# Performance work log

Measured on AMD Instinct MI355X. Metric: run time of the kernel, lower is better.

The kernel has to match this reference:

```python
import jax, jax.numpy as jnp
import numpy as np

N = 50000          # nodes
E = 800000         # edges per meta-path (avg degree 16)
M = 2              # meta-paths
IN = 256           # in_size
H, D = 4, 64       # heads, out_size per head
HD = H * D
SEM_HID = 128      # SemanticAttention hidden_size
NEG_SLOPE = 0.2    # DGL GATConv default LeakyReLU slope


def setup_inputs() -> dict:
    key = jax.random.key(0)
    ks = jax.random.split(key, 10)
    h = jax.random.normal(ks[0], (N, IN), dtype=jnp.float32)
    src = jax.random.randint(ks[1], (M, E), 0, N, dtype=jnp.int32)
    dst = jax.random.randint(ks[2], (M, E), 0, N, dtype=jnp.int32)
    # per-meta-path GATConv params
    W = jax.random.normal(ks[3], (M, IN, HD), dtype=jnp.float32) * (1.0 / np.sqrt(IN))
    attn_l = jax.random.normal(ks[4], (M, H, D), dtype=jnp.float32) * 0.1
    attn_r = jax.random.normal(ks[5], (M, H, D), dtype=jnp.float32) * 0.1
    # semantic attention params
    sem_w1 = jax.random.normal(ks[6], (HD, SEM_HID), dtype=jnp.float32) * (1.0 / np.sqrt(HD))
    sem_b1 = jnp.zeros((SEM_HID,), dtype=jnp.float32)
    sem_w2 = jax.random.normal(ks[7], (SEM_HID, 1), dtype=jnp.float32) * (1.0 / np.sqrt(SEM_HID))
    return {"h": h, "src": src, "dst": dst, "W": W, "attn_l": attn_l,
            "attn_r": attn_r, "sem_w1": sem_w1, "sem_b1": sem_b1, "sem_w2": sem_w2}


def _gat_conv(h, s, d, W_i, al, ar):
    # h: [N, IN]; s, d: [E] int edge endpoints; returns [N, H*D]
    feat = (h @ W_i).reshape(N, H, D)                       # [N,H,D]
    el = jnp.einsum('nhd,hd->nh', feat, al)                 # [N,H]
    er = jnp.einsum('nhd,hd->nh', feat, ar)                 # [N,H]
    e = jax.nn.leaky_relu(el[s] + er[d], NEG_SLOPE)         # [E,H]
    # edge softmax over incoming edges of each dst node
    m = jax.ops.segment_max(e, d, num_segments=N)           # [N,H]
    m = jax.lax.stop_gradient(jnp.where(jnp.isfinite(m), m, 0.0))
    ex = jnp.exp(e - m[d])                                  # [E,H]
    den = jax.ops.segment_sum(ex, d, num_segments=N)        # [N,H]
    alpha = ex / jnp.maximum(den[d], 1e-9)                  # [E,H]
    msg = alpha[:, :, None] * feat[s]                       # [E,H,D]
    rst = jax.ops.segment_sum(msg, d, num_segments=N)       # [N,H,D] (zero for 0-in-degree)
    return jax.nn.elu(rst).reshape(N, HD)


def reference(h, src, dst, W, attn_l, attn_r, sem_w1, sem_b1, sem_w2):
    embs = [_gat_conv(h, src[i], dst[i], W[i], attn_l[i], attn_r[i]) for i in range(M)]
    z = jnp.stack(embs, axis=1)                             # [N,M,HD]
    # semantic attention: w = mean over nodes of MLP score per meta-path
    w = jnp.einsum('nms,so->mo', jnp.tanh(jnp.einsum('nmd,ds->nms', z, sem_w1) + sem_b1), sem_w2) / N  # [M,1]
    beta = jax.nn.softmax(w, axis=0)                        # [M,1]
    return jnp.einsum('nmd,mo->nd', z, beta)                # [N,HD]
```

## Files before the change

kernel.cpp:

```cpp
#include <hip/hip_runtime.h>
#include <hip/hip_bf16.h>

#define NND 50000
#define NE 800000
#define NM 2
#define INF 256
#define NH 4
#define HDIM 256
#define SHID 128
#define SLOPE 0.2f
#define NB 196
#define NREP 8

typedef unsigned short u16;
typedef __attribute__((ext_vector_type(8))) short bf16x8;
typedef __attribute__((ext_vector_type(4))) float f32x4;

__device__ __forceinline__ float us2f(u16 u) {
  union { unsigned int i; float f; } v; v.i = ((unsigned int)u) << 16; return v.f;
}
__device__ __forceinline__ u16 f2us(float f) {
  union { float f; unsigned int i; } v; v.f = f;
  unsigned int r = v.i + 0x7FFFu + ((v.i >> 16) & 1u);
  return (u16)(r >> 16);
}

#define GLDS(g, l) __builtin_amdgcn_global_load_lds( \
    (const __attribute__((address_space(1))) unsigned int*)(g), \
    (__attribute__((address_space(3))) unsigned int*)(l), 16, 0, 0)

__global__ __launch_bounds__(256) void kprep(
    const float* __restrict__ h, u16* __restrict__ hb,
    const float* __restrict__ W, u16* __restrict__ Wt,
    const float* __restrict__ w1, u16* __restrict__ w1t)
{
  __shared__ u16 tile[64][65];
  const int t = threadIdx.x;
  const int bid = blockIdx.x;
  if (bid < 6250) {
    const size_t i = ((size_t)bid * 256 + t) * 8;
    float4 a = *(const float4*)(h + i);
    float4 b = *(const float4*)(h + i + 4);
    bf16x8 r;
    r[0] = f2us(a.x); r[1] = f2us(a.y); r[2] = f2us(a.z); r[3] = f2us(a.w);
    r[4] = f2us(b.x); r[5] = f2us(b.y); r[6] = f2us(b.z); r[7] = f2us(b.w);
    *(bf16x8*)(hb + i) = r;
  } else if (bid < 6250 + 32) {
    const int b = bid - 6250;
    const int k0 = (b & 3) * 64, n0 = ((b >> 2) & 3) * 64;
    const float* Wm = W + (size_t)(b >> 4) * 65536;
    u16* Wtm = Wt + (size_t)(b >> 4) * 65536;
    const int lr = t >> 2, c0 = (t & 3) * 16;
#pragma unroll
    for (int i = 0; i < 16; ++i)
      tile[lr][c0 + i] = f2us(Wm[(size_t)(k0 + lr) * 256 + n0 + c0 + i]);
    __syncthreads();
#pragma unroll
    for (int i = 0; i < 16; ++i)
      Wtm[(size_t)(n0 + lr) * 256 + k0 + c0 + i] = tile[c0 + i][lr];
  } else {
    const int b = bid - 6282;
    const int k0 = (b & 3) * 64, j0 = (b >> 2) * 64;
    const int lr = t >> 2, c0 = (t & 3) * 16;
#pragma unroll
    for (int i = 0; i < 16; ++i)
      tile[lr][c0 + i] = f2us(w1[(size_t)(k0 + lr) * SHID + j0 + c0 + i]);
    __syncthreads();
#pragma unroll
    for (int i = 0; i < 16; ++i)
      w1t[(size_t)(j0 + lr) * 256 + k0 + c0 + i] = tile[c0 + i][lr];
  }
}

__global__ __launch_bounds__(256) void kc_hist_both(const int* __restrict__ dst_all,
                                                    int* __restrict__ hrep) {
  int e = blockIdx.x * 256 + threadIdx.x;
  int p = (e >= NE) ? 1 : 0;
  int rep = blockIdx.x & (NREP - 1);
  atomicAdd(hrep + ((size_t)p * NREP + rep) * (NND + 1) + dst_all[e] + 1, 1);
}

__global__ __launch_bounds__(256) void ks1(const int* __restrict__ hrep,
                                           int* __restrict__ rowptr,
                                           int* __restrict__ bsum) {
  __shared__ int wsums[4];
  const int t = threadIdx.x;
  const int p = blockIdx.x / NB, lb = blockIdx.x % NB;
  int* rp = rowptr + (size_t)p * (NND + 1);
  const int i = lb * 256 + t + 1;
  int v = 0;
  if (i <= NND) {
    const int* hp = hrep + (size_t)p * NREP * (NND + 1);
#pragma unroll
    for (int r = 0; r < NREP; ++r) v += hp[(size_t)r * (NND + 1) + i];
  }
  const int lane = t & 63, wid = t >> 6;
#pragma unroll
  for (int o = 1; o < 64; o <<= 1) {
    int u = __shfl_up(v, o, 64);
    if (lane >= o) v += u;
  }
  if (lane == 63) wsums[wid] = v;
  __syncthreads();
  if (t == 0) {
    int s = 0;
#pragma unroll
    for (int w = 0; w < 4; ++w) { int x = wsums[w]; wsums[w] = s; s += x; }
    bsum[blockIdx.x] = s;
  }
  __syncthreads();
  v += wsums[wid];
  if (i <= NND) rp[i] = v;
}

__global__ __launch_bounds__(256) void ks3(int* __restrict__ rowptr,
                                           const int* __restrict__ bsum,
                                           int* __restrict__ cursor) {
  __shared__ int redp[4];
  __shared__ int off_s;
  const int t = threadIdx.x;
  const int p = blockIdx.x / NB, lb = blockIdx.x % NB;
  int* rp = rowptr + (size_t)p * (NND + 1);
  int* cp = cursor + (size_t)p * NND;
  int partial = (t < lb) ? bsum[p * NB + t] : 0;
  const int lane = t & 63, wid = t >> 6;
#pragma unroll
  for (int o = 32; o; o >>= 1) partial += __shfl_xor(partial, o, 64);
  if (lane == 0) redp[wid] = partial;
  __syncthreads();
  if (t == 0) off_s = redp[0] + redp[1] + redp[2] + redp[3];
  __syncthreads();
  const int off = off_s;
  const int i = lb * 256 + t + 1;
  if (i <= NND) {
    int v = rp[i] + off;
    rp[i] = v;
    if (i < NND) cp[i] = v;
    if (i == 1) { cp[0] = 0; rp[0] = 0; }
  }
}

__global__ __launch_bounds__(256) void kc_scatter(
    const int* __restrict__ src, const int* __restrict__ dst,
    int* __restrict__ cursor, int* __restrict__ col,
    const float* __restrict__ el, const float* __restrict__ er,
    float* __restrict__ exps)
{
  int e = blockIdx.x * 256 + threadIdx.x;
  if (e >= NE) return;
  int s = src[e], d = dst[e];
  int pos = atomicAdd(cursor + d, 1);
  col[pos] = s;
  float4 a = *(const float4*)(el + s * 4);
  float4 b = *(const float4*)(er + d * 4);
  float4 r;
  float x;
  x = a.x + b.x; x = x > 0.f ? x : SLOPE * x; r.x = __expf(x);
  x = a.y + b.y; x = x > 0.f ? x : SLOPE * x; r.y = __expf(x);
  x = a.z + b.z; x = x > 0.f ? x : SLOPE * x; r.z = __expf(x);
  x = a.w + b.w; x = x > 0.f ? x : SLOPE * x; r.w = __expf(x);
  *(float4*)(exps + (size_t)pos * 4) = r;
}

__global__ __launch_bounds__(256) void k1_mfma(
    const u16* __restrict__ hb, const u16* __restrict__ Wt,
    const float* __restrict__ al, const float* __restrict__ ar,
    u16* __restrict__ feat, float* __restrict__ el, float* __restrict__ er)
{
  __shared__ u16 As[128 * 64];
  __shared__ u16 Bs[128 * 64];
  const int t = threadIdx.x;
  const int lane = t & 63;
  const int w = t >> 6;
  const int wr = w >> 1, wc = w & 1;
  const int row0 = blockIdx.x * 128;
  const int col0 = blockIdx.y * 128;

  const int srow = t >> 3;
  const int sg   = t & 7;
  const int sgl  = (sg ^ (srow & 7)) * 8;

  int ra[4], cb[4];
#pragma unroll
  for (int q = 0; q < 4; ++q) {
    int r = row0 + q * 32 + srow; if (r >= NND) r = NND - 1;
    ra[q] = r;
    cb[q] = col0 + q * 32 + srow;
  }

  f32x4 acc[4][4];
#pragma unroll
  for (int i = 0; i < 4; ++i)
#pragma unroll
    for (int j = 0; j < 4; ++j) acc[i][j] = (f32x4){0.f, 0.f, 0.f, 0.f};

  for (int ks = 0; ks < 4; ++ks) {
    const int kb = ks * 64 + sgl;
    __syncthreads();
#pragma unroll
    for (int q = 0; q < 4; ++q) {
      GLDS(hb + (size_t)ra[q] * INF + kb, As + q * 2048 + w * 512);
      GLDS(Wt + (size_t)cb[q] * 256 + kb, Bs + q * 2048 + w * 512);
    }
    __syncthreads();
#pragma unroll
    for (int kk = 0; kk < 2; ++kk) {
      bf16x8 af[4], bfr[4];
#pragma unroll
      for (int mi = 0; mi < 4; ++mi) {
        const int R = wr * 64 + mi * 16 + (lane & 15);
        const int g = kk * 4 + (lane >> 4);
        af[mi] = *(const bf16x8*)(As + R * 64 + (g ^ (R & 7)) * 8);
      }
#pragma unroll
      for (int ni = 0; ni < 4; ++ni) {
        const int R = wc * 64 + ni * 16 + (lane & 15);
        const int g = kk * 4 + (lane >> 4);
        bfr[ni] = *(const bf16x8*)(Bs + R * 64 + (g ^ (R & 7)) * 8);
      }
#pragma unroll
      for (int mi = 0; mi < 4; ++mi)
#pragma unroll
        for (int ni = 0; ni < 4; ++ni)
          acc[mi][ni] = __builtin_amdgcn_mfma_f32_16x16x32_bf16(af[mi], bfr[ni], acc[mi][ni], 0, 0, 0);
    }
  }
  const int head = (col0 >> 6) + wc;
  float alc[4], arc[4];
#pragma unroll
  for (int ni = 0; ni < 4; ++ni) {
    const int c = col0 + wc * 64 + ni * 16 + (lane & 15);
    alc[ni] = al[c]; arc[ni] = ar[c];
  }
#pragma unroll
  for (int mi = 0; mi < 4; ++mi) {
#pragma unroll
    for (int i = 0; i < 4; ++i) {
      const int r = row0 + wr * 64 + mi * 16 + (lane >> 4) * 4 + i;
      const bool valid = (r < NND);
      float pel = 0.f, per = 0.f;
#pragma unroll
      for (int ni = 0; ni < 4; ++ni) {
        const float fe = acc[mi][ni][i];
        if (valid)
          feat[(size_t)r * HDIM + col0 + wc * 64 + ni * 16 + (lane & 15)] = f2us(fe);
        pel = fmaf(fe, alc[ni], pel);
        per = fmaf(fe, arc[ni], per);
      }
#pragma unroll
      for (int o = 1; o < 16; o <<= 1) {
        pel += __shfl_xor(pel, o, 64);
        per += __shfl_xor(per, o, 64);
      }
      if (valid && (lane & 15) == 0) {
        el[r * 4 + head] = pel;
        er[r * 4 + head] = per;
      }
    }
  }
}

template<int OBF>
__global__ __launch_bounds__(256) void k3_gather(
    const int* __restrict__ rowptr, const int* __restrict__ col,
    const float* __restrict__ exps,
    const u16* __restrict__ feat, void* __restrict__ z)
{
  const int d = blockIdx.x * 4 + (threadIdx.x >> 6);
  if (d >= NND) return;
  const int lane = threadIdx.x & 63;
  const int h = lane >> 4;
  const int sub = lane & 15;
  const int beg = rowptr[d], end = rowptr[d + 1];

  float den = 0.f;
  for (int j = beg + sub; j < end; j += 16)
    den += exps[(size_t)j * 4 + h];
#pragma unroll
  for (int o = 1; o < 16; o <<= 1) den += __shfl_xor(den, o, 64);
  const float inv = 1.f / fmaxf(den, 1e-9f);

  float a0 = 0.f, a1 = 0.f, a2 = 0.f, a3 = 0.f;
  int j = beg;
  for (; j + 3 < end; j += 4) {
    int s0 = col[j], s1 = col[j + 1], s2 = col[j + 2], s3 = col[j + 3];
    float p0 = exps[(size_t)j * 4 + h] * inv;
    float p1 = exps[(size_t)(j + 1) * 4 + h] * inv;
    float p2 = exps[(size_t)(j + 2) * 4 + h] * inv;
    float p3 = exps[(size_t)(j + 3) * 4 + h] * inv;
    const ushort4 f0 = *(const ushort4*)(feat + (size_t)s0 * HDIM + lane * 4);
    const ushort4 f1 = *(const ushort4*)(feat + (size_t)s1 * HDIM + lane * 4);
    const ushort4 f2 = *(const ushort4*)(feat + (size_t)s2 * HDIM + lane * 4);
    const ushort4 f3 = *(const ushort4*)(feat + (size_t)s3 * HDIM + lane * 4);
    a0 = fmaf(p0, us2f(f0.x), a0); a1 = fmaf(p0, us2f(f0.y), a1);
    a2 = fmaf(p0, us2f(f0.z), a2); a3 = fmaf(p0, us2f(f0.w), a3);
    a0 = fmaf(p1, us2f(f1.x), a0); a1 = fmaf(p1, us2f(f1.y), a1);
    a2 = fmaf(p1, us2f(f1.z), a2); a3 = fmaf(p1, us2f(f1.w), a3);
    a0 = fmaf(p2, us2f(f2.x), a0); a1 = fmaf(p2, us2f(f2.y), a1);
    a2 = fmaf(p2, us2f(f2.z), a2); a3 = fmaf(p2, us2f(f2.w), a3);
    a0 = fmaf(p3, us2f(f3.x), a0); a1 = fmaf(p3, us2f(f3.y), a1);
    a2 = fmaf(p3, us2f(f3.z), a2); a3 = fmaf(p3, us2f(f3.w), a3);
  }
  for (; j < end; ++j) {
    int s = col[j];
    float p = exps[(size_t)j * 4 + h] * inv;
    const ushort4 f4 = *(const ushort4*)(feat + (size_t)s * HDIM + lane * 4);
    a0 = fmaf(p, us2f(f4.x), a0); a1 = fmaf(p, us2f(f4.y), a1);
    a2 = fmaf(p, us2f(f4.z), a2); a3 = fmaf(p, us2f(f4.w), a3);
  }
  a0 = a0 > 0.f ? a0 : expf(a0) - 1.f;
  a1 = a1 > 0.f ? a1 : expf(a1) - 1.f;
  a2 = a2 > 0.f ? a2 : expf(a2) - 1.f;
  a3 = a3 > 0.f ? a3 : expf(a3) - 1.f;
  const size_t idx = (size_t)d * HDIM + lane * 4;
  if (OBF) {
    ushort4 r; r.x = f2us(a0); r.y = f2us(a1); r.z = f2us(a2); r.w = f2us(a3);
    *(ushort4*)((u16*)z + idx) = r;
  } else {
    float4 r; r.x = a0; r.y = a1; r.z = a2; r.w = a3;
    *(float4*)((float*)z + idx) = r;
  }
}

template<int ZBF>
__global__ __launch_bounds__(256) void k4_mfma(
    const void* __restrict__ zsrc, const u16* __restrict__ w1t,
    const float* __restrict__ b1, const float* __restrict__ w2,
    float* __restrict__ wsum, int midx)
{
  __shared__ u16 As[128 * 64];
  __shared__ u16 Bs[128 * 64];
  __shared__ float red[4];
  const int t = threadIdx.x;
  const int lane = t & 63;
  const int w = t >> 6;
  const int wr = w >> 1, wc = w & 1;
  const int row0 = blockIdx.x * 128;
  const int srow = t >> 3;
  const int sg   = t & 7;
  const int sgl  = (sg ^ (srow & 7)) * 8;

  int ra[4], cb[4];
#pragma unroll
  for (int q = 0; q < 4; ++q) {
    int r = row0 + q * 32 + srow; if (r >= NND) r = NND - 1;
    ra[q] = r;
    cb[q] = q * 32 + srow;
  }

  f32x4 acc[4][4];
#pragma unroll
  for (int i = 0; i < 4; ++i)
#pragma unroll
    for (int j = 0; j < 4; ++j) acc[i][j] = (f32x4){0.f, 0.f, 0.f, 0.f};

  for (int ks = 0; ks < 4; ++ks) {
    const int kb = ks * 64 + sgl;
    __syncthreads();
    if (ZBF) {
#pragma unroll
      for (int q = 0; q < 4; ++q)
        GLDS((const u16*)zsrc + (size_t)ra[q] * HDIM + kb, As + q * 2048 + w * 512);
    } else {
      const float* zf = (const float*)zsrc;
#pragma unroll
      for (int q = 0; q < 4; ++q) {
        float4 a = *(const float4*)(zf + (size_t)ra[q] * HDIM + kb);
        float4 b = *(const float4*)(zf + (size_t)ra[q] * HDIM + kb + 4);
        bf16x8 r;
        r[0] = f2us(a.x); r[1] = f2us(a.y); r[2] = f2us(a.z); r[3] = f2us(a.w);
        r[4] = f2us(b.x); r[5] = f2us(b.y); r[6] = f2us(b.z); r[7] = f2us(b.w);
        *(bf16x8*)(As + (q * 32 + srow) * 64 + (sg ^ (srow & 7)) * 8) = r;
      }
    }
#pragma unroll
    for (int q = 0; q < 4; ++q)
      GLDS(w1t + (size_t)cb[q] * 256 + kb, Bs + q * 2048 + w * 512);
    __syncthreads();
#pragma unroll
    for (int kk = 0; kk < 2; ++kk) {
      bf16x8 af[4], bfr[4];
#pragma unroll
      for (int mi = 0; mi < 4; ++mi) {
        const int R = wr * 64 + mi * 16 + (lane & 15);
        const int g = kk * 4 + (lane >> 4);
        af[mi] = *(const bf16x8*)(As + R * 64 + (g ^ (R & 7)) * 8);
      }
#pragma unroll
      for (int ni = 0; ni < 4; ++ni) {
        const int R = wc * 64 + ni * 16 + (lane & 15);
        const int g = kk * 4 + (lane >> 4);
        bfr[ni] = *(const bf16x8*)(Bs + R * 64 + (g ^ (R & 7)) * 8);
      }
#pragma unroll
      for (int mi = 0; mi < 4; ++mi)
#pragma unroll
        for (int ni = 0; ni < 4; ++ni)
          acc[mi][ni] = __builtin_amdgcn_mfma_f32_16x16x32_bf16(af[mi], bfr[ni], acc[mi][ni], 0, 0, 0);
    }
  }
  float sum = 0.f;
#pragma unroll
  for (int ni = 0; ni < 4; ++ni) {
    const int c = wc * 64 + ni * 16 + (lane & 15);
    const float b1c = b1[c], w2c = w2[c];
#pragma unroll
    for (int mi = 0; mi < 4; ++mi) {
      const int r_base = row0 + wr * 64 + mi * 16 + (lane >> 4) * 4;
#pragma unroll
      for (int i = 0; i < 4; ++i) {
        if (r_base + i < NND)
          sum += tanhf(acc[mi][ni][i] + b1c) * w2c;
      }
    }
  }
#pragma unroll
  for (int o = 32; o; o >>= 1) sum += __shfl_xor(sum, o, 64);
  if (lane == 0) red[w] = sum;
  __syncthreads();
  if (t == 0) unsafeAtomicAdd(wsum + midx, red[0] + red[1] + red[2] + red[3]);
}

__global__ __launch_bounds__(256) void k5_out(
    float* __restrict__ out, const u16* __restrict__ z1,
    const float* __restrict__ wsum)
{
  const int i = blockIdx.x * 256 + threadIdx.x;
  float w0 = wsum[0] * (1.0f / NND);
  float w1v = wsum[1] * (1.0f / NND);
  float mx = fmaxf(w0, w1v);
  float e0 = expf(w0 - mx), e1 = expf(w1v - mx);
  float inv = 1.f / (e0 + e1);
  float b0 = e0 * inv, b1 = e1 * inv;
  float4 a = ((const float4*)out)[i];
  ushort4 zb = ((const ushort4*)z1)[i];
  float4 r;
  r.x = b0 * a.x + b1 * us2f(zb.x);
  r.y = b0 * a.y + b1 * us2f(zb.y);
  r.z = b0 * a.z + b1 * us2f(zb.z);
  r.w = b0 * a.w + b1 * us2f(zb.w);
  ((float4*)out)[i] = r;
}

extern "C" void kernel_launch(void* const* d_in, const int* in_sizes, int n_in,
                              void* d_out, int out_size, void* d_ws, size_t ws_size,
                              hipStream_t stream)
{
  const float* h  = (const float*)d_in[0];
  const int* src  = (const int*)d_in[1];
  const int* dst  = (const int*)d_in[2];
  const float* W  = (const float*)d_in[3];
  const float* al = (const float*)d_in[4];
  const float* ar = (const float*)d_in[5];
  const float* w1 = (const float*)d_in[6];
  const float* b1 = (const float*)d_in[7];
  const float* w2 = (const float*)d_in[8];

  char* wsb = (char*)d_ws;
  u16*   feat   = (u16*)(wsb);
  u16*   hz     = (u16*)(wsb + 25600000);
  float* exps   = (float*)(wsb + 51200000);
  int*   col    = (int*)(wsb + 64000000);
  u16*   Wt     = (u16*)(wsb + 67200000);
  u16*   w1t    = (u16*)(wsb + 67462144);
  float* el     = (float*)(wsb + 67527680);
  float* er     = (float*)(wsb + 68327680);
  int*   rowptr = (int*)(wsb + 69127680);
  int*   cursor = (int*)(wsb + 69527688);
  float* wsum   = (float*)(wsb + 69927688);
  int*   bsum   = (int*)(wsb + 69927696);
  int*   hrep   = (int*)(wsb + 69929264);
  const size_t NEED = 73129328;
  if (ws_size < NEED) {
    hipMemsetAsync(d_out, 0x7F, (size_t)out_size * 4, stream);
    return;
  }
  u16* z1 = hz;
  float* outp = (float*)d_out;

  kprep<<<6290, 256, 0, stream>>>(h, hz, W, Wt, w1, w1t);
  hipMemsetAsync(wsum, 0, 2 * sizeof(float), stream);
  hipMemsetAsync(hrep, 0, (size_t)2 * NREP * (NND + 1) * sizeof(int), stream);
  kc_hist_both<<<2 * NE / 256, 256, 0, stream>>>(dst, hrep);
  ks1<<<2 * NB, 256, 0, stream>>>(hrep, rowptr, bsum);
  ks3<<<2 * NB, 256, 0, stream>>>(rowptr, bsum, cursor);

  for (int m = 0; m < NM; ++m) {
    const int* src_m = src + (size_t)m * NE;
    const int* dst_m = dst + (size_t)m * NE;
    int* rowptr_m = rowptr + (size_t)m * (NND + 1);
    int* cursor_m = cursor + (size_t)m * NND;
    k1_mfma<<<dim3(391, 2), 256, 0, stream>>>(hz, Wt + (size_t)m * 65536,
                                              al + (size_t)m * HDIM, ar + (size_t)m * HDIM,
                                              feat, el, er);
    kc_scatter<<<NE / 256, 256, 0, stream>>>(src_m, dst_m, cursor_m, col, el, er, exps);
    if (m == 0) {
      k3_gather<0><<<12500, 256, 0, stream>>>(rowptr_m, col, exps, feat, d_out);
      k4_mfma<0><<<391, 256, 0, stream>>>(d_out, w1t, b1, w2, wsum, 0);
    } else {
      k3_gather<1><<<12500, 256, 0, stream>>>(rowptr_m, col, exps, feat, z1);
      k4_mfma<1><<<391, 256, 0, stream>>>(z1, w1t, b1, w2, wsum, 1);
    }
  }
  k5_out<<<(NND * HDIM / 4) / 256, 256, 0, stream>>>(outp, z1, wsum);
}
```

Measured before the change: 414.4 us.

## Widen GEMM tiles to 512-thread blocks, double histogram replicas, fold wsum memset

k1_mfma now computes all 256 output columns per 128-row block with 8 waves, so each A tile is loaded once instead of twice. k4_mfma takes 256 rows per 512-thread block, which halves the number of reloads of the shared w1t tile. The histogram replica count rises from 8 to 16 to cut atomic contention, at the cost of a larger memset and more summing work in ks1. The wsum zeroing moves into ks1, removing one memset launch. The larger tiles raise LDS use and lower the number of blocks in flight.

```diff
diff --git a/kernel.cpp b/kernel.cpp
--- a/kernel.cpp
+++ b/kernel.cpp
@@ -10,7 +10,7 @@
 #define SHID 128
 #define SLOPE 0.2f
 #define NB 196
-#define NREP 8
+#define NREP 16
 
 typedef unsigned short u16;
 typedef __attribute__((ext_vector_type(8))) short bf16x8;
@@ -82,9 +82,11 @@
 
 __global__ __launch_bounds__(256) void ks1(const int* __restrict__ hrep,
                                            int* __restrict__ rowptr,
-                                           int* __restrict__ bsum) {
+                                           int* __restrict__ bsum,
+                                           float* __restrict__ wsum) {
   __shared__ int wsums[4];
   const int t = threadIdx.x;
+  if (blockIdx.x == 0 && t < 2) wsum[t] = 0.f;
   const int p = blockIdx.x / NB, lb = blockIdx.x % NB;
   int* rp = rowptr + (size_t)p * (NND + 1);
   const int i = lb * 256 + t + 1;
@@ -162,31 +164,31 @@
   *(float4*)(exps + (size_t)pos * 4) = r;
 }
 
-__global__ __launch_bounds__(256) void k1_mfma(
+__global__ __launch_bounds__(512) void k1_mfma(
     const u16* __restrict__ hb, const u16* __restrict__ Wt,
     const float* __restrict__ al, const float* __restrict__ ar,
     u16* __restrict__ feat, float* __restrict__ el, float* __restrict__ er)
 {
   __shared__ u16 As[128 * 64];
-  __shared__ u16 Bs[128 * 64];
+  __shared__ u16 Bs[256 * 64];
   const int t = threadIdx.x;
   const int lane = t & 63;
   const int w = t >> 6;
-  const int wr = w >> 1, wc = w & 1;
+  const int wr = w >> 2, wc = w & 3;
   const int row0 = blockIdx.x * 128;
-  const int col0 = blockIdx.y * 128;
 
   const int srow = t >> 3;
   const int sg   = t & 7;
   const int sgl  = (sg ^ (srow & 7)) * 8;
 
-  int ra[4], cb[4];
-#pragma unroll
-  for (int q = 0; q < 4; ++q) {
-    int r = row0 + q * 32 + srow; if (r >= NND) r = NND - 1;
+  int ra[2], cb[4];
+#pragma unroll
+  for (int q = 0; q < 2; ++q) {
+    int r = row0 + q * 64 + srow; if (r >= NND) r = NND - 1;
     ra[q] = r;
-    cb[q] = col0 + q * 32 + srow;
-  }
+  }
+#pragma unroll
+  for (int q = 0; q < 4; ++q) cb[q] = q * 64 + srow;
 
   f32x4 acc[4][4];
 #pragma unroll
@@ -198,10 +200,11 @@
     const int kb = ks * 64 + sgl;
     __syncthreads();
 #pragma unroll
-    for (int q = 0; q < 4; ++q) {
-      GLDS(hb + (size_t)ra[q] * INF + kb, As + q * 2048 + w * 512);
-      GLDS(Wt + (size_t)cb[q] * 256 + kb, Bs + q * 2048 + w * 512);
-    }
+    for (int q = 0; q < 2; ++q)
+      GLDS(hb + (size_t)ra[q] * INF + kb, As + q * 4096 + w * 512);
+#pragma unroll
+    for (int q = 0; q < 4; ++q)
+      GLDS(Wt + (size_t)cb[q] * 256 + kb, Bs + q * 4096 + w * 512);
     __syncthreads();
 #pragma unroll
     for (int kk = 0; kk < 2; ++kk) {
@@ -225,11 +228,11 @@
           acc[mi][ni] = __builtin_amdgcn_mfma_f32_16x16x32_bf16(af[mi], bfr[ni], acc[mi][ni], 0, 0, 0);
     }
   }
-  const int head = (col0 >> 6) + wc;
+  const int head = wc;
   float alc[4], arc[4];
 #pragma unroll
   for (int ni = 0; ni < 4; ++ni) {
-    const int c = col0 + wc * 64 + ni * 16 + (lane & 15);
+    const int c = wc * 64 + ni * 16 + (lane & 15);
     alc[ni] = al[c]; arc[ni] = ar[c];
   }
 #pragma unroll
@@ -243,7 +246,7 @@
       for (int ni = 0; ni < 4; ++ni) {
         const float fe = acc[mi][ni][i];
         if (valid)
-          feat[(size_t)r * HDIM + col0 + wc * 64 + ni * 16 + (lane & 15)] = f2us(fe);
+          feat[(size_t)r * HDIM + wc * 64 + ni * 16 + (lane & 15)] = f2us(fe);
         pel = fmaf(fe, alc[ni], pel);
         per = fmaf(fe, arc[ni], per);
       }
@@ -323,30 +326,31 @@
 }
 
 template<int ZBF>
-__global__ __launch_bounds__(256) void k4_mfma(
+__global__ __launch_bounds__(512) void k4_mfma(
     const void* __restrict__ zsrc, const u16* __restrict__ w1t,
     const float* __restrict__ b1, const float* __restrict__ w2,
     float* __restrict__ wsum, int midx)
 {
-  __shared__ u16 As[128 * 64];
+  __shared__ u16 As[256 * 64];
   __shared__ u16 Bs[128 * 64];
-  __shared__ float red[4];
+  __shared__ float red[8];
   const int t = threadIdx.x;
   const int lane = t & 63;
   const int w = t >> 6;
   const int wr = w >> 1, wc = w & 1;
-  const int row0 = blockIdx.x * 128;
+  const int row0 = blockIdx.x * 256;
   const int srow = t >> 3;
   const int sg   = t & 7;
   const int sgl  = (sg ^ (srow & 7)) * 8;
 
-  int ra[4], cb[4];
+  int ra[4], cb[2];
 #pragma unroll
   for (int q = 0; q < 4; ++q) {
-    int r = row0 + q * 32 + srow; if (r >= NND) r = NND - 1;
+    int r = row0 + q * 64 + srow; if (r >= NND) r = NND - 1;
     ra[q] = r;
-    cb[q] = q * 32 + srow;
-  }
+  }
+#pragma unroll
+  for (int q = 0; q < 2; ++q) cb[q] = q * 64 + srow;
 
   f32x4 acc[4][4];
 #pragma unroll
@@ -360,7 +364,7 @@
     if (ZBF) {
 #pragma unroll
       for (int q = 0; q < 4; ++q)
-        GLDS((const u16*)zsrc + (size_t)ra[q] * HDIM + kb, As + q * 2048 + w * 512);
+        GLDS((const u16*)zsrc + (size_t)ra[q] * HDIM + kb, As + q * 4096 + w * 512);
     } else {
       const float* zf = (const float*)zsrc;
 #pragma unroll
@@ -370,12 +374,12 @@
         bf16x8 r;
         r[0] = f2us(a.x); r[1] = f2us(a.y); r[2] = f2us(a.z); r[3] = f2us(a.w);
         r[4] = f2us(b.x); r[5] = f2us(b.y); r[6] = f2us(b.z); r[7] = f2us(b.w);
-        *(bf16x8*)(As + (q * 32 + srow) * 64 + (sg ^ (srow & 7)) * 8) = r;
+        *(bf16x8*)(As + (q * 64 + srow) * 64 + (sg ^ (srow & 7)) * 8) = r;
       }
     }
 #pragma unroll
-    for (int q = 0; q < 4; ++q)
-      GLDS(w1t + (size_t)cb[q] * 256 + kb, Bs + q * 2048 + w * 512);
+    for (int q = 0; q < 2; ++q)
+      GLDS(w1t + (size_t)cb[q] * 256 + kb, Bs + q * 4096 + w * 512);
     __syncthreads();
 #pragma unroll
     for (int kk = 0; kk < 2; ++kk) {
@@ -418,7 +422,12 @@
   for (int o = 32; o; o >>= 1) sum += __shfl_xor(sum, o, 64);
   if (lane == 0) red[w] = sum;
   __syncthreads();
-  if (t == 0) unsafeAtomicAdd(wsum + midx, red[0] + red[1] + red[2] + red[3]);
+  if (t == 0) {
+    float s = 0.f;
+#pragma unroll
+    for (int q = 0; q < 8; ++q) s += red[q];
+    unsafeAtomicAdd(wsum + midx, s);
+  }
 }
 
 __global__ __launch_bounds__(256) void k5_out(
@@ -470,7 +479,7 @@
   float* wsum   = (float*)(wsb + 69927688);
   int*   bsum   = (int*)(wsb + 69927696);
   int*   hrep   = (int*)(wsb + 69929264);
-  const size_t NEED = 73129328;
+  const size_t NEED = 76329392;
   if (ws_size < NEED) {
     hipMemsetAsync(d_out, 0x7F, (size_t)out_size * 4, stream);
     return;
@@ -479,10 +488,9 @@
   float* outp = (float*)d_out;
 
   kprep<<<6290, 256, 0, stream>>>(h, hz, W, Wt, w1, w1t);
-  hipMemsetAsync(wsum, 0, 2 * sizeof(float), stream);
   hipMemsetAsync(hrep, 0, (size_t)2 * NREP * (NND + 1) * sizeof(int), stream);
   kc_hist_both<<<2 * NE / 256, 256, 0, stream>>>(dst, hrep);
-  ks1<<<2 * NB, 256, 0, stream>>>(hrep, rowptr, bsum);
+  ks1<<<2 * NB, 256, 0, stream>>>(hrep, rowptr, bsum, wsum);
   ks3<<<2 * NB, 256, 0, stream>>>(rowptr, bsum, cursor);
 
   for (int m = 0; m < NM; ++m) {
@@ -490,16 +498,16 @@
     const int* dst_m = dst + (size_t)m * NE;
     int* rowptr_m = rowptr + (size_t)m * (NND + 1);
     int* cursor_m = cursor + (size_t)m * NND;
-    k1_mfma<<<dim3(391, 2), 256, 0, stream>>>(hz, Wt + (size_t)m * 65536,
-                                              al + (size_t)m * HDIM, ar + (size_t)m * HDIM,
-                                              feat, el, er);
+    k1_mfma<<<391, 512, 0, stream>>>(hz, Wt + (size_t)m * 65536,
+                                     al + (size_t)m * HDIM, ar + (size_t)m * HDIM,
+                                     feat, el, er);
     kc_scatter<<<NE / 256, 256, 0, stream>>>(src_m, dst_m, cursor_m, col, el, er, exps);
     if (m == 0) {
       k3_gather<0><<<12500, 256, 0, stream>>>(rowptr_m, col, exps, feat, d_out);
-      k4_mfma<0><<<391, 256, 0, stream>>>(d_out, w1t, b1, w2, wsum, 0);
+      k4_mfma<0><<<196, 512, 0, stream>>>(d_out, w1t, b1, w2, wsum, 0);
     } else {
       k3_gather<1><<<12500, 256, 0, stream>>>(rowptr_m, col, exps, feat, z1);
-      k4_mfma<1><<<391, 256, 0, stream>>>(z1, w1t, b1, w2, wsum, 1);
+      k4_mfma<1><<<196, 512, 0, stream>>>(z1, w1t, b1, w2, wsum, 1);
     }
   }
   k5_out<<<(NND * HDIM / 4) / 256, 256, 0, stream>>>(outp, z1, wsum);
```

After: 397.1 us. 4.2% less time.
